# Optimization experiments

Hardware: AMD Instinct MI355X
Metric: run time of the kernel (lower is better)

Reference implementation:

```python
import jax, jax.numpy as jnp
import numpy as np

S = 2   # scale_factor
K = 5   # k_up
M = 48  # m_channels
KE = 3  # k_encoder


def conv2d(x, w, b, pad):
    # NCHW conv, stride 1, symmetric padding (matches nn.Conv2d(padding=pad))
    y = jax.lax.conv_general_dilated(
        x, w, window_strides=(1, 1), padding=[(pad, pad), (pad, pad)],
        dimension_numbers=("NCHW", "OIHW", "NCHW"))
    return y + b[None, :, None, None]


def setup_inputs() -> dict:
    key = jax.random.key(0)
    k1, k2, k3, k4, k5 = jax.random.split(key, 5)
    C_in = 64
    x = jax.random.normal(k1, (8, C_in, 128, 128), dtype=jnp.float32)
    w_compress = jax.random.normal(k2, (M, C_in, 1, 1), dtype=jnp.float32) * 0.1
    b_compress = jax.random.normal(k3, (M,), dtype=jnp.float32) * 0.05
    w_encoder = jax.random.normal(k4, ((K * S) ** 2, M, KE, KE), dtype=jnp.float32) * 0.05
    b_encoder = jax.random.normal(k5, ((K * S) ** 2,), dtype=jnp.float32) * 0.05
    return {"x": x, "w_compress": w_compress, "b_compress": b_compress,
            "w_encoder": w_encoder, "b_encoder": b_encoder}


def reference(x, w_compress, b_compress, w_encoder, b_encoder):
    B, C, H, W = x.shape
    # mask branch: compress -> relu -> encoder -> softmax over k_up^2
    y = jax.nn.relu(conv2d(x, w_compress, b_compress, pad=0))
    y = conv2d(y, w_encoder, b_encoder, pad=KE // 2)          # [B, (K*S)^2, H, W]
    y = y.reshape(B, S * S, K * K, H, W)
    y = jax.nn.softmax(y, axis=2)
    # unfold x with kernel K, pad K//2, stride 1 -> [B, C, K*K, H, W]
    p = K // 2
    xpad = jnp.pad(x, ((0, 0), (0, 0), (p, p), (p, p)))
    unf = jnp.stack([xpad[:, :, i:i + H, j:j + W]
                     for i in range(K) for j in range(K)], axis=2)
    # per-subpixel softmax-weighted patch sum; channel layout (scale_idx, C)
    out = jnp.einsum("bskhw,bckhw->bschw", y, unf)            # [B, S^2, C, H, W]
    out = out.reshape(B, S * S * C, H, W)
    # PixelShuffle(S): view (B, C_out, r, r, H, W) -> (B, C_out, H, r, W, r)
    r = S
    c_out = (S * S * C) // (r * r)
    out = out.reshape(B, c_out, r, r, H, W).transpose(0, 1, 4, 2, 5, 3)
    return out.reshape(B, c_out, H * r, W * r)
```

## Files before the change

### kernel.cpp

```cpp
#include <hip/hip_runtime.h>

#define HW 16384

typedef __bf16 bf16x8 __attribute__((ext_vector_type(8)));
typedef __bf16 bf16x4 __attribute__((ext_vector_type(4)));
typedef float  f32x4  __attribute__((ext_vector_type(4)));
typedef float  f32x2  __attribute__((ext_vector_type(2)));

__global__ __launch_bounds__(256)
void prep_w(const float* __restrict__ we, const float* __restrict__ wc,
            __bf16* __restrict__ wt, __bf16* __restrict__ wcb) {
    int idx = blockIdx.x * 256 + threadIdx.x;
    if (idx < 128 * 448) {
        int e = idx / 448, k = idx % 448;
        float v = 0.f;
        if (e < 100 && k < 432) {
            int t = k / 48, m = k % 48;
            v = we[(e * 48 + m) * 9 + t];
        }
        wt[idx] = (__bf16)v;
    } else {
        idx -= 128 * 448;
        if (idx < 48 * 64) wcb[idx] = (__bf16)wc[idx];
    }
}

__global__ __launch_bounds__(256, 2)
void prep_xty1(const float* __restrict__ x, const __bf16* __restrict__ wcb,
               const float* __restrict__ bc,
               __bf16* __restrict__ xt, __bf16* __restrict__ y1o) {
    __shared__ __align__(16) float lds[256 * 65];
    __bf16* y1s = (__bf16*)lds;

    const int b = blockIdx.x & 7, chunk = blockIdx.x >> 3;
    const int t = threadIdx.x;
    const int lane = t & 63, wv = t >> 6;
    const int lgp = lane >> 4, lr = lane & 15;
    const int pos0 = chunk * 256;

    const float* xb = x + (size_t)b * 64 * HW + pos0;
    for (int c = 0; c < 64; ++c)
        lds[t * 65 + c] = xb[(size_t)c * HW + t];
    __syncthreads();

    {
        const int q = t & 3, pp = t >> 2;
        #pragma unroll
        for (int it = 0; it < 4; ++it) {
            int pos = it * 64 + pp;
            __bf16* o = xt + ((size_t)b * HW + pos0 + pos) * 64 + q * 16;
            bf16x8 v0, v1;
            #pragma unroll
            for (int e = 0; e < 8; ++e) {
                v0[e] = (__bf16)lds[pos * 65 + q * 16 + e];
                v1[e] = (__bf16)lds[pos * 65 + q * 16 + 8 + e];
            }
            *(bf16x8*)o       = v0;
            *(bf16x8*)(o + 8) = v1;
        }
    }
    bf16x8 af[4][2];
    #pragma unroll
    for (int i = 0; i < 4; ++i) {
        int pix = (wv * 4 + i) * 16 + lr;
        #pragma unroll
        for (int kc = 0; kc < 2; ++kc)
            #pragma unroll
            for (int e = 0; e < 8; ++e)
                af[i][kc][e] = (__bf16)lds[pix * 65 + kc * 32 + lgp * 8 + e];
    }
    __syncthreads();

    {
        bf16x8 bw[3][2];
        f32x4 bias4[3];
        #pragma unroll
        for (int nt = 0; nt < 3; ++nt) {
            bias4[nt] = *(const f32x4*)(bc + nt * 16 + lgp * 4);
            #pragma unroll
            for (int kc = 0; kc < 2; ++kc)
                bw[nt][kc] = *(const bf16x8*)(wcb + (nt * 16 + lr) * 64 + kc * 32 + lgp * 8);
        }
        #pragma unroll
        for (int i = 0; i < 4; ++i) {
            int pix = (wv * 4 + i) * 16 + lr;
            #pragma unroll
            for (int nt = 0; nt < 3; ++nt) {
                f32x4 cc = bias4[nt];
                cc = __builtin_amdgcn_mfma_f32_16x16x32_bf16(bw[nt][0], af[i][0], cc, 0, 0, 0);
                cc = __builtin_amdgcn_mfma_f32_16x16x32_bf16(bw[nt][1], af[i][1], cc, 0, 0, 0);
                bf16x4 o4;
                #pragma unroll
                for (int r = 0; r < 4; ++r) o4[r] = (__bf16)fmaxf(cc[r], 0.f);
                *(bf16x4*)(y1s + pix * 56 + nt * 16 + lgp * 4) = o4;
            }
        }
    }
    __syncthreads();

    __bf16* yo = y1o + (size_t)(b * HW + pos0) * 48;
    #pragma unroll
    for (int i = 0; i < 6; ++i) {
        int c = i * 256 + t;
        int pix = (c * 10923) >> 16;
        int mc  = c - pix * 6;
        bf16x8 v = *(bf16x8*)(y1s + pix * 56 + mc * 8);
        *(bf16x8*)(yo + (size_t)c * 8) = v;
    }
}

__global__ __launch_bounds__(256, 2)
void carafe_wa(const __bf16* __restrict__ xt, const __bf16* __restrict__ y1g,
               const __bf16* __restrict__ wt, const float* __restrict__ be,
               float* __restrict__ out) {
    __shared__ __align__(16) char smem[60416];
    __bf16*    y1  = (__bf16*)smem;
    _Float16*  lgt = (_Float16*)smem;
    __bf16*    lx  = (__bf16*)smem;

    const int tid = threadIdx.x;
    const int lane = tid & 63, wv = tid >> 6;
    const int lgp = lane >> 4, lr = lane & 15;
    const int b = blockIdx.x & 7, tile = blockIdx.x >> 3;
    const int h0 = (tile >> 3) << 4, w0 = (tile & 7) << 4;

    const __bf16* y1b = y1g + (size_t)b * HW * 48;
    #pragma unroll
    for (int it = 0; it < 8; ++it) {
        int id = it * 256 + tid;
        if (id < 1944) {
            int hr  = (id * 607) >> 16;
            int rem = id - hr * 108;
            int wc  = (rem * 10923) >> 16;
            int mc  = rem - wc * 6;
            int hy = h0 - 1 + hr, wx = w0 - 1 + wc;
            bf16x8 v = {};
            if (hy >= 0 && hy < 128 && wx >= 0 && wx < 128)
                v = *(const bf16x8*)(y1b + (size_t)(hy * 128 + wx) * 48 + mc * 8);
            *(bf16x8*)(y1 + (hr * 18 + wc) * 56 + mc * 8) = v;
        }
    }
    for (int i = tid; i < 1120; i += 256)
        y1[324 * 56 + i] = (__bf16)0.f;
    __syncthreads();

    f32x4 acc[4][7];
    #pragma unroll
    for (int ot = 0; ot < 7; ++ot) {
        int o_ = ot * 16 + lr;
        float bz = (o_ < 100) ? be[o_] : 0.f;
        #pragma unroll
        for (int i = 0; i < 4; ++i) acc[i][ot] = {bz, bz, bz, bz};
    }
    const int ptg0 = wv * 4;

    auto ldA = [&](bf16x8 A[4], int kc) {
        int Kb = kc * 32 + lgp * 8;
        int t  = (Kb * 683) >> 15;  int m0 = Kb - t * 48;
        int ty = (t * 11) >> 5;     int tx = t - ty * 3;
        int base = ty * 18 + lr + tx;
        #pragma unroll
        for (int i = 0; i < 4; ++i)
            A[i] = *(const bf16x8*)(y1 + ((ptg0 + i) * 18 + base) * 56 + m0);
    };
    auto ldB = [&](bf16x8 B[7], int kc) {
        #pragma unroll
        for (int j = 0; j < 7; ++j)
            B[j] = *(const bf16x8*)(wt + (j * 16 + lr) * 448 + kc * 32 + lgp * 8);
    };
    auto mm = [&](bf16x8 A[4], bf16x8 B[7]) {
        #pragma unroll
        for (int i = 0; i < 4; ++i)
            #pragma unroll
            for (int j = 0; j < 7; ++j)
                acc[i][j] = __builtin_amdgcn_mfma_f32_16x16x32_bf16(A[i], B[j], acc[i][j], 0, 0, 0);
    };

    bf16x8 A0[4], B0[7], A1[4], B1[7];
    ldA(A0, 0); ldB(B0, 0);
    #pragma unroll
    for (int kc = 0; kc < 14; kc += 2) {
        if (kc + 1 < 14) { ldA(A1, kc + 1); ldB(B1, kc + 1); }
        mm(A0, B0);
        if (kc + 2 < 14) { ldA(A0, kc + 2); ldB(B0, kc + 2); }
        if (kc + 1 < 14) mm(A1, B1);
    }
    __syncthreads();

    #pragma unroll
    for (int i = 0; i < 4; ++i)
        #pragma unroll
        for (int j = 0; j < 7; ++j) {
            int o_ = j * 16 + lr;
            #pragma unroll
            for (int r = 0; r < 4; ++r) {
                int p = (ptg0 + i) * 16 + lgp * 4 + r;
                lgt[p * 118 + o_] = (_Float16)acc[i][j][r];
            }
        }

    bf16x8 hv[13];
    #pragma unroll
    for (int it = 0; it < 13; ++it) {
        int id = it * 256 + tid;
        bf16x8 v = {};
        if (id < 3200) {
            int pos = id >> 3, l8 = id & 7;
            int r = pos / 20, q = pos % 20;
            int hy = h0 - 2 + r, wx = w0 - 2 + q;
            if (hy >= 0 && hy < 128 && wx >= 0 && wx < 128)
                v = *(const bf16x8*)(xt + ((size_t)b * HW + hy * 128 + wx) * 64 + l8 * 8);
        }
        hv[it] = v;
    }
    __syncthreads();

    const int py = tid >> 4, px = tid & 15;
    const int h = h0 + py, w = w0 + px;
    float wt_[100];
    {
        const _Float16* lrow = lgt + tid * 118;
        #pragma unroll
        for (int g = 0; g < 4; ++g) {
            float* v = wt_ + g * 25;
            #pragma unroll
            for (int k = 0; k < 25; ++k) v[k] = (float)lrow[g * 25 + k];
            float mx = v[0];
            #pragma unroll
            for (int k = 1; k < 25; ++k) mx = fmaxf(mx, v[k]);
            float s = 0.f;
            #pragma unroll
            for (int k = 0; k < 25; ++k) { v[k] = __expf(v[k] - mx); s += v[k]; }
            float inv = 1.f / s;
            #pragma unroll
            for (int k = 0; k < 25; ++k) v[k] *= inv;
        }
    }
    __syncthreads();

    #pragma unroll
    for (int it = 0; it < 13; ++it) {
        int id = it * 256 + tid;
        if (id < 3200) {
            int pos = id >> 3, l8 = id & 7;
            bf16x4 vlo = {hv[it][0], hv[it][1], hv[it][2], hv[it][3]};
            bf16x4 vhi = {hv[it][4], hv[it][5], hv[it][6], hv[it][7]};
            *(bf16x4*)(lx + pos * 68 + l8 * 8)     = vlo;
            *(bf16x4*)(lx + pos * 68 + l8 * 8 + 4) = vhi;
        }
    }
    __syncthreads();

    float* ob = out + (size_t)b * 256 * HW;
    #pragma unroll 1
    for (int cq = 0; cq < 16; ++cq) {
        f32x2 g0l = {0.f, 0.f}, g0h = {0.f, 0.f}, g1l = {0.f, 0.f}, g1h = {0.f, 0.f};
        f32x2 g2l = {0.f, 0.f}, g2h = {0.f, 0.f}, g3l = {0.f, 0.f}, g3h = {0.f, 0.f};
        #pragma unroll
        for (int ki = 0; ki < 5; ++ki) {
            const int rowbase = (py + ki) * 20 + px;
            #pragma unroll
            for (int kj = 0; kj < 5; ++kj) {
                uint2 u = *(const uint2*)(lx + (rowbase + kj) * 68 + cq * 4);
                f32x2 xlo = { __uint_as_float(u.x << 16), __uint_as_float(u.x & 0xffff0000u) };
                f32x2 xhi = { __uint_as_float(u.y << 16), __uint_as_float(u.y & 0xffff0000u) };
                const int k = ki * 5 + kj;
                float w0_ = wt_[k], w1_ = wt_[25 + k], w2_ = wt_[50 + k], w3_ = wt_[75 + k];
                g0l += xlo * w0_;  g0h += xhi * w0_;
                g1l += xlo * w1_;  g1h += xhi * w1_;
                g2l += xlo * w2_;  g2h += xhi * w2_;
                g3l += xlo * w3_;  g3h += xhi * w3_;
            }
        }
        const size_t pstride = (size_t)16 * 256 * 256;
        size_t base = ((size_t)cq * 256 + 2 * h) * 256 + 2 * w;
        __builtin_nontemporal_store(g0l, (f32x2*)(ob + base));
        __builtin_nontemporal_store(g0h, (f32x2*)(ob + base + 256));
        __builtin_nontemporal_store(g1l, (f32x2*)(ob + base + pstride));
        __builtin_nontemporal_store(g1h, (f32x2*)(ob + base + pstride + 256));
        __builtin_nontemporal_store(g2l, (f32x2*)(ob + base + 2 * pstride));
        __builtin_nontemporal_store(g2h, (f32x2*)(ob + base + 2 * pstride + 256));
        __builtin_nontemporal_store(g3l, (f32x2*)(ob + base + 3 * pstride));
        __builtin_nontemporal_store(g3h, (f32x2*)(ob + base + 3 * pstride + 256));
    }
}

extern "C" void kernel_launch(void* const* d_in, const int* in_sizes, int n_in,
                              void* d_out, int out_size, void* d_ws, size_t ws_size,
                              hipStream_t stream) {
    const float* x  = (const float*)d_in[0];
    const float* wc = (const float*)d_in[1];
    const float* bc = (const float*)d_in[2];
    const float* we = (const float*)d_in[3];
    const float* be = (const float*)d_in[4];
    float* out = (float*)d_out;

    __bf16* xt  = (__bf16*)d_ws;
    __bf16* y1g = (__bf16*)((char*)d_ws + 16777216);
    __bf16* wte = (__bf16*)((char*)d_ws + 41943040);
    __bf16* wcb = (__bf16*)((char*)d_ws + 41943040 + 114688);

    prep_w<<<236, 256, 0, stream>>>(we, wc, wte, wcb);
    prep_xty1<<<512, 256, 0, stream>>>(x, wcb, bc, xt, y1g);
    carafe_wa<<<512, 256, 0, stream>>>(xt, y1g, wte, be, out);
}
```

Baseline: 79.69 us.

## Fuse weight prep into xty1 kernel and halve CARAFE tile height

The encoder-weight transpose is folded into the first prep kernel as extra blocks, and the compress weights are converted from fp32 inside each block instead of in a separate pass, which drops one launch. The main kernel now uses 8x16 pixel tiles with 1024 blocks. Each thread handles one pixel and two of the four subpixel groups, which shrinks LDS to about 32KB and the register arrays, so launch bounds can target 4 blocks per CU. The trade-off is more halo overhead per tile, since a 3-row halo for the encoder and 4 rows for the unfold are reloaded over only 8 rows. Each block also now holds the dependency of the wt buffer on prep blocks in the same launch, which is fine because the next kernel runs after it.

```diff
diff --git a/kernel.cpp b/kernel.cpp
--- a/kernel.cpp
+++ b/kernel.cpp
@@ -7,33 +7,27 @@
 typedef float  f32x4  __attribute__((ext_vector_type(4)));
 typedef float  f32x2  __attribute__((ext_vector_type(2)));
 
-__global__ __launch_bounds__(256)
-void prep_w(const float* __restrict__ we, const float* __restrict__ wc,
-            __bf16* __restrict__ wt, __bf16* __restrict__ wcb) {
-    int idx = blockIdx.x * 256 + threadIdx.x;
-    if (idx < 128 * 448) {
+__global__ __launch_bounds__(256, 2)
+void prep_fused(const float* __restrict__ x, const float* __restrict__ we,
+                const float* __restrict__ wc, const float* __restrict__ bc,
+                __bf16* __restrict__ xt, __bf16* __restrict__ y1o,
+                __bf16* __restrict__ wt) {
+    const int t = threadIdx.x;
+    if (blockIdx.x >= 512) {
+        int idx = (blockIdx.x - 512) * 256 + t;
         int e = idx / 448, k = idx % 448;
         float v = 0.f;
         if (e < 100 && k < 432) {
-            int t = k / 48, m = k % 48;
-            v = we[(e * 48 + m) * 9 + t];
+            int tt = k / 48, m = k % 48;
+            v = we[(e * 48 + m) * 9 + tt];
         }
         wt[idx] = (__bf16)v;
-    } else {
-        idx -= 128 * 448;
-        if (idx < 48 * 64) wcb[idx] = (__bf16)wc[idx];
-    }
-}
-
-__global__ __launch_bounds__(256, 2)
-void prep_xty1(const float* __restrict__ x, const __bf16* __restrict__ wcb,
-               const float* __restrict__ bc,
-               __bf16* __restrict__ xt, __bf16* __restrict__ y1o) {
+        return;
+    }
     __shared__ __align__(16) float lds[256 * 65];
     __bf16* y1s = (__bf16*)lds;
 
     const int b = blockIdx.x & 7, chunk = blockIdx.x >> 3;
-    const int t = threadIdx.x;
     const int lane = t & 63, wv = t >> 6;
     const int lgp = lane >> 4, lr = lane & 15;
     const int pos0 = chunk * 256;
@@ -78,8 +72,15 @@
         for (int nt = 0; nt < 3; ++nt) {
             bias4[nt] = *(const f32x4*)(bc + nt * 16 + lgp * 4);
             #pragma unroll
-            for (int kc = 0; kc < 2; ++kc)
-                bw[nt][kc] = *(const bf16x8*)(wcb + (nt * 16 + lr) * 64 + kc * 32 + lgp * 8);
+            for (int kc = 0; kc < 2; ++kc) {
+                f32x4 w0 = *(const f32x4*)(wc + (nt * 16 + lr) * 64 + kc * 32 + lgp * 8);
+                f32x4 w1 = *(const f32x4*)(wc + (nt * 16 + lr) * 64 + kc * 32 + lgp * 8 + 4);
+                #pragma unroll
+                for (int e = 0; e < 4; ++e) {
+                    bw[nt][kc][e]     = (__bf16)w0[e];
+                    bw[nt][kc][e + 4] = (__bf16)w1[e];
+                }
+            }
         }
         #pragma unroll
         for (int i = 0; i < 4; ++i) {
@@ -109,11 +110,11 @@
     }
 }
 
-__global__ __launch_bounds__(256, 2)
+__global__ __launch_bounds__(256, 4)
 void carafe_wa(const __bf16* __restrict__ xt, const __bf16* __restrict__ y1g,
                const __bf16* __restrict__ wt, const float* __restrict__ be,
                float* __restrict__ out) {
-    __shared__ __align__(16) char smem[60416];
+    __shared__ __align__(16) char smem[32640];
     __bf16*    y1  = (__bf16*)smem;
     _Float16*  lgt = (_Float16*)smem;
     __bf16*    lx  = (__bf16*)smem;
@@ -122,13 +123,13 @@
     const int lane = tid & 63, wv = tid >> 6;
     const int lgp = lane >> 4, lr = lane & 15;
     const int b = blockIdx.x & 7, tile = blockIdx.x >> 3;
-    const int h0 = (tile >> 3) << 4, w0 = (tile & 7) << 4;
+    const int h0 = (tile >> 3) << 3, w0 = (tile & 7) << 4;
 
     const __bf16* y1b = y1g + (size_t)b * HW * 48;
     #pragma unroll
-    for (int it = 0; it < 8; ++it) {
+    for (int it = 0; it < 5; ++it) {
         int id = it * 256 + tid;
-        if (id < 1944) {
+        if (id < 1080) {
             int hr  = (id * 607) >> 16;
             int rem = id - hr * 108;
             int wc  = (rem * 10923) >> 16;
@@ -141,26 +142,26 @@
         }
     }
     for (int i = tid; i < 1120; i += 256)
-        y1[324 * 56 + i] = (__bf16)0.f;
-    __syncthreads();
-
-    f32x4 acc[4][7];
+        y1[180 * 56 + i] = (__bf16)0.f;
+    __syncthreads();
+
+    f32x4 acc[2][7];
     #pragma unroll
     for (int ot = 0; ot < 7; ++ot) {
         int o_ = ot * 16 + lr;
         float bz = (o_ < 100) ? be[o_] : 0.f;
         #pragma unroll
-        for (int i = 0; i < 4; ++i) acc[i][ot] = {bz, bz, bz, bz};
-    }
-    const int ptg0 = wv * 4;
-
-    auto ldA = [&](bf16x8 A[4], int kc) {
+        for (int i = 0; i < 2; ++i) acc[i][ot] = {bz, bz, bz, bz};
+    }
+    const int ptg0 = wv * 2;
+
+    auto ldA = [&](bf16x8 A[2], int kc) {
         int Kb = kc * 32 + lgp * 8;
         int t  = (Kb * 683) >> 15;  int m0 = Kb - t * 48;
         int ty = (t * 11) >> 5;     int tx = t - ty * 3;
         int base = ty * 18 + lr + tx;
         #pragma unroll
-        for (int i = 0; i < 4; ++i)
+        for (int i = 0; i < 2; ++i)
             A[i] = *(const bf16x8*)(y1 + ((ptg0 + i) * 18 + base) * 56 + m0);
     };
     auto ldB = [&](bf16x8 B[7], int kc) {
@@ -168,15 +169,15 @@
         for (int j = 0; j < 7; ++j)
             B[j] = *(const bf16x8*)(wt + (j * 16 + lr) * 448 + kc * 32 + lgp * 8);
     };
-    auto mm = [&](bf16x8 A[4], bf16x8 B[7]) {
-        #pragma unroll
-        for (int i = 0; i < 4; ++i)
+    auto mm = [&](bf16x8 A[2], bf16x8 B[7]) {
+        #pragma unroll
+        for (int i = 0; i < 2; ++i)
             #pragma unroll
             for (int j = 0; j < 7; ++j)
                 acc[i][j] = __builtin_amdgcn_mfma_f32_16x16x32_bf16(A[i], B[j], acc[i][j], 0, 0, 0);
     };
 
-    bf16x8 A0[4], B0[7], A1[4], B1[7];
+    bf16x8 A0[2], B0[7], A1[2], B1[7];
     ldA(A0, 0); ldB(B0, 0);
     #pragma unroll
     for (int kc = 0; kc < 14; kc += 2) {
@@ -188,7 +189,7 @@
     __syncthreads();
 
     #pragma unroll
-    for (int i = 0; i < 4; ++i)
+    for (int i = 0; i < 2; ++i)
         #pragma unroll
         for (int j = 0; j < 7; ++j) {
             int o_ = j * 16 + lr;
@@ -199,14 +200,15 @@
             }
         }
 
-    bf16x8 hv[13];
-    #pragma unroll
-    for (int it = 0; it < 13; ++it) {
+    bf16x8 hv[8];
+    #pragma unroll
+    for (int it = 0; it < 8; ++it) {
         int id = it * 256 + tid;
         bf16x8 v = {};
-        if (id < 3200) {
+        if (id < 1920) {
             int pos = id >> 3, l8 = id & 7;
-            int r = pos / 20, q = pos % 20;
+            int r = (pos * 3277) >> 16;
+            int q = pos - r * 20;
             int hy = h0 - 2 + r, wx = w0 - 2 + q;
             if (hy >= 0 && hy < 128 && wx >= 0 && wx < 128)
                 v = *(const bf16x8*)(xt + ((size_t)b * HW + hy * 128 + wx) * 64 + l8 * 8);
@@ -215,13 +217,14 @@
     }
     __syncthreads();
 
-    const int py = tid >> 4, px = tid & 15;
+    const int pix = tid & 127, sgrp = tid >> 7;
+    const int py = pix >> 4, px = pix & 15;
     const int h = h0 + py, w = w0 + px;
-    float wt_[100];
+    float wt_[50];
     {
-        const _Float16* lrow = lgt + tid * 118;
-        #pragma unroll
-        for (int g = 0; g < 4; ++g) {
+        const _Float16* lrow = lgt + pix * 118 + sgrp * 50;
+        #pragma unroll
+        for (int g = 0; g < 2; ++g) {
             float* v = wt_ + g * 25;
             #pragma unroll
             for (int k = 0; k < 25; ++k) v[k] = (float)lrow[g * 25 + k];
@@ -239,9 +242,9 @@
     __syncthreads();
 
     #pragma unroll
-    for (int it = 0; it < 13; ++it) {
+    for (int it = 0; it < 8; ++it) {
         int id = it * 256 + tid;
-        if (id < 3200) {
+        if (id < 1920) {
             int pos = id >> 3, l8 = id & 7;
             bf16x4 vlo = {hv[it][0], hv[it][1], hv[it][2], hv[it][3]};
             bf16x4 vhi = {hv[it][4], hv[it][5], hv[it][6], hv[it][7]};
@@ -254,8 +257,7 @@
     float* ob = out + (size_t)b * 256 * HW;
     #pragma unroll 1
     for (int cq = 0; cq < 16; ++cq) {
-        f32x2 g0l = {0.f, 0.f}, g0h = {0.f, 0.f}, g1l = {0.f, 0.f}, g1h = {0.f, 0.f};
-        f32x2 g2l = {0.f, 0.f}, g2h = {0.f, 0.f}, g3l = {0.f, 0.f}, g3h = {0.f, 0.f};
+        f32x2 a0 = {0.f, 0.f}, a1 = {0.f, 0.f}, a2 = {0.f, 0.f}, a3 = {0.f, 0.f};
         #pragma unroll
         for (int ki = 0; ki < 5; ++ki) {
             const int rowbase = (py + ki) * 20 + px;
@@ -264,24 +266,20 @@
                 uint2 u = *(const uint2*)(lx + (rowbase + kj) * 68 + cq * 4);
                 f32x2 xlo = { __uint_as_float(u.x << 16), __uint_as_float(u.x & 0xffff0000u) };
                 f32x2 xhi = { __uint_as_float(u.y << 16), __uint_as_float(u.y & 0xffff0000u) };
-                const int k = ki * 5 + kj;
-                float w0_ = wt_[k], w1_ = wt_[25 + k], w2_ = wt_[50 + k], w3_ = wt_[75 + k];
-                g0l += xlo * w0_;  g0h += xhi * w0_;
-                g1l += xlo * w1_;  g1h += xhi * w1_;
-                g2l += xlo * w2_;  g2h += xhi * w2_;
-                g3l += xlo * w3_;  g3h += xhi * w3_;
-            }
-        }
-        const size_t pstride = (size_t)16 * 256 * 256;
-        size_t base = ((size_t)cq * 256 + 2 * h) * 256 + 2 * w;
-        __builtin_nontemporal_store(g0l, (f32x2*)(ob + base));
-        __builtin_nontemporal_store(g0h, (f32x2*)(ob + base + 256));
-        __builtin_nontemporal_store(g1l, (f32x2*)(ob + base + pstride));
-        __builtin_nontemporal_store(g1h, (f32x2*)(ob + base + pstride + 256));
-        __builtin_nontemporal_store(g2l, (f32x2*)(ob + base + 2 * pstride));
-        __builtin_nontemporal_store(g2h, (f32x2*)(ob + base + 2 * pstride + 256));
-        __builtin_nontemporal_store(g3l, (f32x2*)(ob + base + 3 * pstride));
-        __builtin_nontemporal_store(g3h, (f32x2*)(ob + base + 3 * pstride + 256));
+                float wA = wt_[ki * 5 + kj];
+                float wB = wt_[25 + ki * 5 + kj];
+                a0 += xlo * wA;
+                a1 += xhi * wA;
+                a2 += xlo * wB;
+                a3 += xhi * wB;
+            }
+        }
+        size_t base0 = ((size_t)(sgrp * 32 + cq) * 256 + 2 * h) * 256 + 2 * w;
+        size_t base1 = base0 + (size_t)16 * 256 * 256;
+        __builtin_nontemporal_store(a0, (f32x2*)(ob + base0));
+        __builtin_nontemporal_store(a1, (f32x2*)(ob + base0 + 256));
+        __builtin_nontemporal_store(a2, (f32x2*)(ob + base1));
+        __builtin_nontemporal_store(a3, (f32x2*)(ob + base1 + 256));
     }
 }
 
@@ -298,9 +296,7 @@
     __bf16* xt  = (__bf16*)d_ws;
     __bf16* y1g = (__bf16*)((char*)d_ws + 16777216);
     __bf16* wte = (__bf16*)((char*)d_ws + 41943040);
-    __bf16* wcb = (__bf16*)((char*)d_ws + 41943040 + 114688);
-
-    prep_w<<<236, 256, 0, stream>>>(we, wc, wte, wcb);
-    prep_xty1<<<512, 256, 0, stream>>>(x, wcb, bc, xt, y1g);
-    carafe_wa<<<512, 256, 0, stream>>>(xt, y1g, wte, be, out);
+
+    prep_fused<<<512 + 224, 256, 0, stream>>>(x, we, wc, bc, xt, y1g, wte);
+    carafe_wa<<<1024, 256, 0, stream>>>(xt, y1g, wte, be, out);
 }
```

Measured after the change: 101.1 us. 26.9% more time.
